# Kernel optimization log

Measured on AMD Instinct MI355X. Metric: run time of the kernel, lower is better.

## Reference

```python
import jax, jax.numpy as jnp
import numpy as np

B, S, D_IN, D_OUT = 8, 4096, 1280, 1280
K1, K2, K3 = 4, 8, 40  # svd_l[1280]


def setup_inputs() -> dict:
    key = jax.random.key(0)
    kx, k1, k2, k3, kw = jax.random.split(key, 5)
    return {
        "x": jax.random.normal(kx, (B, S, D_IN), dtype=jnp.float32),
        "kron_1": jax.random.normal(k1, (K1, K1), dtype=jnp.float32),
        "kron_2": jax.random.normal(k2, (K2, K2), dtype=jnp.float32),
        "kron_3": jax.random.normal(k3, (K3, K3), dtype=jnp.float32),
        "W": jax.random.normal(kw, (D_OUT, D_IN), dtype=jnp.float32) * 0.02,
    }


def _cayley(A):
    # Q = (I - skew) @ inv(I + skew), skew = 0.5*(A - A^T)
    n = A.shape[0]
    skew = 0.5 * (A - A.T)
    I = jnp.eye(n, dtype=A.dtype)
    return (I - skew) @ jnp.linalg.inv(I + skew)


def reference(x, kron_1, kron_2, kron_3, W):
    q1 = _cayley(kron_1)
    q2 = _cayley(kron_2)
    q3 = _cayley(kron_3)
    # R: [in, in] nested Kronecker of the three orthogonal factors
    R = jnp.kron(jnp.kron(q1, q2), q3)
    # filt = (R @ W^T)^T = W @ R^T  -> [out, in]
    filt = (R @ W.T).T
    # linear(x, filt): x @ filt^T  -> [B, S, out]
    return jnp.einsum("bsi,oi->bso", x, filt)
```

## Files before the change

### kernel.cpp

```cpp
#include <hip/hip_runtime.h>
#include <stdint.h>

#define D_IN 1280

typedef __attribute__((ext_vector_type(8))) short s16x8;
typedef __attribute__((ext_vector_type(4))) float f32x4;
typedef __attribute__((ext_vector_type(4))) unsigned int u32x4;

__device__ __forceinline__ unsigned short f2bf(float f) {
  union { float f; unsigned u; } v;
  v.f = f;
  unsigned u = v.u;
  return (unsigned short)((u + 0x7fffu + ((u >> 16) & 1u)) >> 16);
}

__device__ __forceinline__ unsigned int cvtpk(float lo, float hi) {
  unsigned int r;
  asm("v_cvt_pk_bf16_f32 %0, %1, %2" : "=v"(r) : "v"(lo), "v"(hi));
  return r;
}

__device__ __forceinline__ void gload_lds16(const void* g, void* l) {
  __builtin_amdgcn_global_load_lds(
      (const __attribute__((address_space(1))) void*)g,
      (__attribute__((address_space(3))) void*)l, 16, 0, 0);
}

__global__ void cayley_kernel(const float* __restrict__ A1,
                              const float* __restrict__ A2,
                              const float* __restrict__ A3,
                              float* __restrict__ qws) {
  const int which = blockIdx.x;
  const float* __restrict__ A = which == 0 ? A1 : (which == 1 ? A2 : A3);
  float* __restrict__ Q = which == 0 ? qws : (which == 1 ? qws + 16 : qws + 80);
  const int n = which == 0 ? 4 : (which == 1 ? 8 : 40);
  const int t = threadIdx.x;

  __shared__ float aug[40][80];
  __shared__ float Nm[40][40];
  __shared__ float fac[40];

  for (int idx = t; idx < n * n; idx += 256) {
    int i = idx / n, j = idx % n;
    float s = 0.5f * (A[i * n + j] - A[j * n + i]);
    float eye = (i == j) ? 1.0f : 0.0f;
    aug[i][j] = eye + s;
    aug[i][n + j] = eye;
    Nm[i][j] = eye - s;
  }
  __syncthreads();

  for (int p = 0; p < n; ++p) {
    const float d = aug[p][p];
    if (t < n) fac[t] = (t == p) ? 0.0f : aug[t][p];
    __syncthreads();
    const float inv = 1.0f / d;
    if (t < 2 * n) aug[p][t] *= inv;
    __syncthreads();
    for (int idx = t; idx < n * 2 * n; idx += 256) {
      int i = idx / (2 * n), j = idx % (2 * n);
      aug[i][j] -= fac[i] * aug[p][j];
    }
    __syncthreads();
  }

  for (int idx = t; idx < n * n; idx += 256) {
    int i = idx / n, j = idx % n;
    float acc = 0.0f;
    for (int k = 0; k < n; ++k) acc += Nm[i][k] * aug[k][n + j];
    Q[i * n + j] = acc;
  }
}

#define FROWS 4
__global__ __launch_bounds__(320) void filt_kernel(const float* __restrict__ W,
                                                   const float* __restrict__ qws,
                                                   unsigned short* __restrict__ filt) {
  __shared__ float q1s[16];
  __shared__ float q2s[64];
  __shared__ float w[FROWS][D_IN];
  __shared__ float t1[FROWS][D_IN];
  __shared__ float t2[FROWS][D_IN];
  const int t = threadIdx.x;
  const int ob = blockIdx.x * FROWS;

  if (t < 16) q1s[t] = qws[t];
  if (t < 64) q2s[t] = qws[16 + t];

  const int i3 = t % 40;
  const int g = t / 40;
  float q3c[40];
#pragma unroll
  for (int j3 = 0; j3 < 40; ++j3) q3c[j3] = qws[80 + i3 * 40 + j3];

  for (int k = t; k < FROWS * 320; k += 320) {
    int r = k / 320, c = k % 320;
    ((float4*)w[r])[c] = ((const float4*)(W + (size_t)(ob + r) * D_IN))[c];
  }
  __syncthreads();

#pragma unroll
  for (int kk = 0; kk < 16; ++kk) {
    const int item = g * 16 + kk;
    const int r = item >> 5;
    const int b = (item & 31) * 40;
    float s = 0.0f;
#pragma unroll
    for (int j3 = 0; j3 < 40; ++j3) s += w[r][b + j3] * q3c[j3];
    t1[r][b + i3] = s;
  }
  __syncthreads();

  for (int e = t; e < FROWS * D_IN; e += 320) {
    const int r = e / D_IN;
    const int i = e - r * D_IN;
    const int ii3 = i % 40;
    const int i2 = (i / 40) & 7;
    const int j1 = i / 320;
    float s = 0.0f;
#pragma unroll
    for (int j2 = 0; j2 < 8; ++j2) s += q2s[i2 * 8 + j2] * t1[r][j1 * 320 + j2 * 40 + ii3];
    t2[r][i] = s;
  }
  __syncthreads();

  for (int e = t; e < FROWS * D_IN; e += 320) {
    const int r = e / D_IN;
    const int i = e - r * D_IN;
    const int lo = i % 320;
    const int i1 = i / 320;
    float s = 0.0f;
#pragma unroll
    for (int j1 = 0; j1 < 4; ++j1) s += q1s[i1 * 4 + j1] * t2[r][j1 * 320 + lo];
    filt[(size_t)(ob + r) * D_IN + i] = f2bf(s);
  }
}

__global__ __launch_bounds__(256) void cvt_kernel(const float* __restrict__ x,
                                                  unsigned short* __restrict__ xb) {
  const size_t i = ((size_t)blockIdx.x * 256 + threadIdx.x) * 8;
  float4 a = *(const float4*)(x + i);
  float4 b = *(const float4*)(x + i + 4);
  u32x4 p;
  p[0] = cvtpk(a.x, a.y);
  p[1] = cvtpk(a.z, a.w);
  p[2] = cvtpk(b.x, b.y);
  p[3] = cvtpk(b.z, b.w);
  *(u32x4*)(xb + i) = p;
}

__global__ __launch_bounds__(512, 2) void gemm8p_kernel(
    const unsigned short* __restrict__ xb,
    const unsigned short* __restrict__ filt,
    float* __restrict__ out) {
  __shared__ short As[2][2][128][64];
  __shared__ short Bs[2][2][128][64];

  const int t = threadIdx.x;
  const int lane = t & 63;
  const int wave = t >> 6;
  const int wr = wave >> 2;
  const int wc = wave & 3;
  const int hb = wc >> 1;
  const int nloc = (wc & 1) * 64;

  const int nwg = gridDim.x;
  const int bid = blockIdx.x;
  const int wg = (bid & 7) * (nwg >> 3) + (bid >> 3);
  const int mt = wg / 5;
  const int nt = wg % 5;
  const int mbase = mt * 256;
  const int nbase = nt * 256;

  f32x4 acc[8][4];
#pragma unroll
  for (int m = 0; m < 8; ++m)
#pragma unroll
    for (int n = 0; n < 4; ++n) acc[m][n] = 0.0f;

  const int tr = t >> 3;
  const int scol = (((t & 7) ^ (tr & 7)) << 3);
  const int pslot = (t & 7) << 3;
  const unsigned short* __restrict__ abase = xb + (size_t)mbase * D_IN + scol;
  const unsigned short* __restrict__ bbase = filt + (size_t)nbase * D_IN + scol;

#define STAGE_A(P, H, KT)                                                     \
  {                                                                           \
    _Pragma("unroll")                                                         \
    for (int q = 0; q < 2; ++q)                                               \
      gload_lds16(abase + (size_t)((H)*128 + q * 64 + tr) * D_IN + (KT)*64,   \
                  (void*)&As[P][H][q * 64 + tr][pslot]);                      \
  }
#define STAGE_B(P, H, KT)                                                     \
  {                                                                           \
    _Pragma("unroll")                                                         \
    for (int q = 0; q < 2; ++q)                                               \
      gload_lds16(bbase + (size_t)((H)*128 + q * 64 + tr) * D_IN + (KT)*64,   \
                  (void*)&Bs[P][H][q * 64 + tr][pslot]);                      \
  }

  const int lr = lane & 15;
  const int hk = lane >> 4;
  const int c0 = ((hk ^ (lr & 7)) << 3);
  const int c1 = c0 ^ 32;

#define BAR asm volatile("s_barrier" ::: "memory")
#define LGKM0 asm volatile("s_waitcnt lgkmcnt(0)" ::: "memory")

  STAGE_A(0, 0, 0); STAGE_A(0, 1, 0);
  STAGE_B(0, 0, 0); STAGE_B(0, 1, 0);
  STAGE_A(1, 0, 1);
  asm volatile("s_waitcnt vmcnt(2)" ::: "memory");
  BAR;

  s16x8 aLo[8], aHi[8], bLo[4], bHi[4];

#pragma unroll 2
  for (int j = 0; j < 20; ++j) {
    const int d = j & 1;

#pragma unroll
    for (int m = 0; m < 4; ++m) {
      aLo[m * 2 + 0] = *(const s16x8*)&As[d][wr][m * 16 + lr][c0];
      aLo[m * 2 + 1] = *(const s16x8*)&As[d][wr][m * 16 + lr][c1];
    }
#pragma unroll
    for (int n = 0; n < 2; ++n) {
      bLo[n * 2 + 0] = *(const s16x8*)&Bs[d][hb][nloc + n * 16 + lr][c0];
      bLo[n * 2 + 1] = *(const s16x8*)&Bs[d][hb][nloc + n * 16 + lr][c1];
    }
    if (j < 19) STAGE_A(d ^ 1, 1, j + 1);
    BAR; LGKM0;
    __builtin_amdgcn_s_setprio(1);
#pragma unroll
    for (int m = 0; m < 4; ++m)
#pragma unroll
      for (int n = 0; n < 2; ++n)
#pragma unroll
        for (int kk = 0; kk < 2; ++kk)
          acc[m][n] = __builtin_amdgcn_mfma_f32_16x16x32_bf16(
              aLo[m * 2 + kk], bLo[n * 2 + kk], acc[m][n], 0, 0, 0);
    __builtin_amdgcn_s_setprio(0);
    BAR;

#pragma unroll
    for (int n = 0; n < 2; ++n) {
      bHi[n * 2 + 0] = *(const s16x8*)&Bs[d][hb][nloc + (n + 2) * 16 + lr][c0];
      bHi[n * 2 + 1] = *(const s16x8*)&Bs[d][hb][nloc + (n + 2) * 16 + lr][c1];
    }
    if (j < 19) STAGE_B(d ^ 1, 0, j + 1);
    BAR; LGKM0;
    __builtin_amdgcn_s_setprio(1);
#pragma unroll
    for (int m = 0; m < 4; ++m)
#pragma unroll
      for (int n = 0; n < 2; ++n)
#pragma unroll
        for (int kk = 0; kk < 2; ++kk)
          acc[m][n + 2] = __builtin_amdgcn_mfma_f32_16x16x32_bf16(
              aLo[m * 2 + kk], bHi[n * 2 + kk], acc[m][n + 2], 0, 0, 0);
    __builtin_amdgcn_s_setprio(0);
    BAR;

#pragma unroll
    for (int m = 0; m < 4; ++m) {
      aHi[m * 2 + 0] = *(const s16x8*)&As[d][wr][(m + 4) * 16 + lr][c0];
      aHi[m * 2 + 1] = *(const s16x8*)&As[d][wr][(m + 4) * 16 + lr][c1];
    }
    if (j < 19) STAGE_B(d ^ 1, 1, j + 1);
    BAR; LGKM0;
    __builtin_amdgcn_s_setprio(1);
#pragma unroll
    for (int m = 0; m < 4; ++m)
#pragma unroll
      for (int n = 0; n < 2; ++n)
#pragma unroll
        for (int kk = 0; kk < 2; ++kk)
          acc[m + 4][n + 2] = __builtin_amdgcn_mfma_f32_16x16x32_bf16(
              aHi[m * 2 + kk], bHi[n * 2 + kk], acc[m + 4][n + 2], 0, 0, 0);
    __builtin_amdgcn_s_setprio(0);
    BAR;

    if (j < 18) STAGE_A(d, 0, j + 2);
    BAR;
    __builtin_amdgcn_s_setprio(1);
#pragma unroll
    for (int m = 0; m < 4; ++m)
#pragma unroll
      for (int n = 0; n < 2; ++n)
#pragma unroll
        for (int kk = 0; kk < 2; ++kk)
          acc[m + 4][n] = __builtin_amdgcn_mfma_f32_16x16x32_bf16(
              aHi[m * 2 + kk], bLo[n * 2 + kk], acc[m + 4][n], 0, 0, 0);
    __builtin_amdgcn_s_setprio(0);
    if (j <= 17)      asm volatile("s_waitcnt vmcnt(2)" ::: "memory");
    else if (j == 18) asm volatile("s_waitcnt vmcnt(0)" ::: "memory");
    BAR;
  }
#undef STAGE_A
#undef STAGE_B
#undef BAR
#undef LGKM0

  const int orow = (lane >> 4) << 2;
  const int ocol = lane & 15;
#pragma unroll
  for (int m = 0; m < 8; ++m) {
#pragma unroll
    for (int r = 0; r < 4; ++r) {
      float* cp = out + (size_t)(mbase + wr * 128 + m * 16 + orow + r) * D_IN +
                  nbase + wc * 64 + ocol;
#pragma unroll
      for (int n = 0; n < 4; ++n) cp[n * 16] = acc[m][n][r];
    }
  }
}

__global__ __launch_bounds__(256) void gemm_fb_kernel(const float* __restrict__ x,
                                                      const unsigned short* __restrict__ filt,
                                                      float* __restrict__ out) {
  __shared__ short As[128][32];
  __shared__ short Bs[128][32];

  const int t = threadIdx.x;
  const int lane = t & 63;
  const int wave = t >> 6;
  const int wr = wave >> 1;
  const int wc = wave & 1;

  const int nwg = gridDim.x;
  const int bid = blockIdx.x;
  const int wg = (bid & 7) * (nwg >> 3) + (bid >> 3);
  const int mt = wg / 10;
  const int nt = wg % 10;
  const int mbase = mt * 128;
  const int nbase = nt * 128;

  f32x4 acc[4][4];
#pragma unroll
  for (int m = 0; m < 4; ++m)
#pragma unroll
    for (int n = 0; n < 4; ++n) acc[m][n] = 0.0f;

  const int ar = t >> 1;
  const int ac = (t & 1) << 4;
  const float* __restrict__ asrc = x + (size_t)(mbase + ar) * D_IN + ac;

  const int br = t >> 2;
  const int bc = (t & 3) << 3;
  const unsigned short* __restrict__ bsrc0 = filt + (size_t)(nbase + br) * D_IN + bc;
  const unsigned short* __restrict__ bsrc1 = filt + (size_t)(nbase + br + 64) * D_IN + bc;
  short* bdst0 = &Bs[br][bc];
  short* bdst1 = &Bs[br + 64][bc];

  const int lr = lane & 15;
  const int lk = (lane >> 4) << 3;

  for (int kt = 0; kt < D_IN; kt += 32) {
    gload_lds16(bsrc0 + kt, bdst0);
    gload_lds16(bsrc1 + kt, bdst1);

    const float* src = asrc + kt;
    float4 f0 = *(const float4*)(src + 0);
    float4 f1 = *(const float4*)(src + 4);
    float4 f2 = *(const float4*)(src + 8);
    float4 f3 = *(const float4*)(src + 12);
    u32x4 p0, p1;
    p0[0] = cvtpk(f0.x, f0.y); p0[1] = cvtpk(f0.z, f0.w);
    p0[2] = cvtpk(f1.x, f1.y); p0[3] = cvtpk(f1.z, f1.w);
    p1[0] = cvtpk(f2.x, f2.y); p1[1] = cvtpk(f2.z, f2.w);
    p1[2] = cvtpk(f3.x, f3.y); p1[3] = cvtpk(f3.z, f3.w);
    *(u32x4*)&As[ar][ac] = p0;
    *(u32x4*)&As[ar][ac + 16] = p1;

    __syncthreads();

    s16x8 a[4], b[4];
#pragma unroll
    for (int m = 0; m < 4; ++m)
      a[m] = *(const s16x8*)&As[wr * 64 + m * 16 + lr][lk];
#pragma unroll
    for (int n = 0; n < 4; ++n)
      b[n] = *(const s16x8*)&Bs[wc * 64 + n * 16 + lr][lk];
#pragma unroll
    for (int m = 0; m < 4; ++m)
#pragma unroll
      for (int n = 0; n < 4; ++n)
        acc[m][n] = __builtin_amdgcn_mfma_f32_16x16x32_bf16(a[m], b[n], acc[m][n], 0, 0, 0);

    __syncthreads();
  }

  const int orow = (lane >> 4) << 2;
  const int ocol = lane & 15;
#pragma unroll
  for (int m = 0; m < 4; ++m) {
#pragma unroll
    for (int r = 0; r < 4; ++r) {
      float* cp = out + (size_t)(mbase + wr * 64 + m * 16 + orow + r) * D_IN +
                  nbase + wc * 64 + ocol;
#pragma unroll
      for (int n = 0; n < 4; ++n) cp[n * 16] = acc[m][n][r];
    }
  }
}

extern "C" void kernel_launch(void* const* d_in, const int* in_sizes, int n_in,
                              void* d_out, int out_size, void* d_ws, size_t ws_size,
                              hipStream_t stream) {
  (void)in_sizes; (void)n_in; (void)out_size;
  const float* x = (const float*)d_in[0];
  const float* k1 = (const float*)d_in[1];
  const float* k2 = (const float*)d_in[2];
  const float* k3 = (const float*)d_in[3];
  const float* W = (const float*)d_in[4];
  float* out = (float*)d_out;

  float* qws = (float*)d_ws;
  unsigned short* filt = (unsigned short*)((char*)d_ws + 8192);
  unsigned short* xb = (unsigned short*)((char*)d_ws + (4u << 20));
  const size_t need = (4ull << 20) + (size_t)32768 * D_IN * 2;

  cayley_kernel<<<3, 256, 0, stream>>>(k1, k2, k3, qws);
  filt_kernel<<<D_IN / FROWS, 320, 0, stream>>>(W, qws, filt);

  if (ws_size >= need) {
    cvt_kernel<<<20480, 256, 0, stream>>>(x, xb);
    gemm8p_kernel<<<640, 512, 0, stream>>>(xb, filt, out);
  } else {
    gemm_fb_kernel<<<2560, 256, 0, stream>>>(x, filt, out);
  }
}
```

Before: 268.3 us.

## Fuse fp32-to-bf16 conversion of x into the GEMM A-tile staging

New measurement: 288.8 us. 7.7% more time.

```diff
diff --git a/kernel.cpp b/kernel.cpp
--- a/kernel.cpp
+++ b/kernel.cpp
@@ -136,21 +136,8 @@
   }
 }
 
-__global__ __launch_bounds__(256) void cvt_kernel(const float* __restrict__ x,
-                                                  unsigned short* __restrict__ xb) {
-  const size_t i = ((size_t)blockIdx.x * 256 + threadIdx.x) * 8;
-  float4 a = *(const float4*)(x + i);
-  float4 b = *(const float4*)(x + i + 4);
-  u32x4 p;
-  p[0] = cvtpk(a.x, a.y);
-  p[1] = cvtpk(a.z, a.w);
-  p[2] = cvtpk(b.x, b.y);
-  p[3] = cvtpk(b.z, b.w);
-  *(u32x4*)(xb + i) = p;
-}
-
 __global__ __launch_bounds__(512, 2) void gemm8p_kernel(
-    const unsigned short* __restrict__ xb,
+    const float* __restrict__ x,
     const unsigned short* __restrict__ filt,
     float* __restrict__ out) {
   __shared__ short As[2][2][128][64];
@@ -181,16 +168,8 @@
   const int tr = t >> 3;
   const int scol = (((t & 7) ^ (tr & 7)) << 3);
   const int pslot = (t & 7) << 3;
-  const unsigned short* __restrict__ abase = xb + (size_t)mbase * D_IN + scol;
   const unsigned short* __restrict__ bbase = filt + (size_t)nbase * D_IN + scol;
 
-#define STAGE_A(P, H, KT)                                                     \
-  {                                                                           \
-    _Pragma("unroll")                                                         \
-    for (int q = 0; q < 2; ++q)                                               \
-      gload_lds16(abase + (size_t)((H)*128 + q * 64 + tr) * D_IN + (KT)*64,   \
-                  (void*)&As[P][H][q * 64 + tr][pslot]);                      \
-  }
 #define STAGE_B(P, H, KT)                                                     \
   {                                                                           \
     _Pragma("unroll")                                                         \
@@ -199,6 +178,32 @@
                   (void*)&Bs[P][H][q * 64 + tr][pslot]);                      \
   }
 
+  const int ar = t >> 2;
+  const int acol = (t & 3) * 16;
+  const int as0 = (t & 3) * 2;
+  const int am = ar & 7;
+  const float* __restrict__ a0base = x + (size_t)(mbase + ar) * D_IN + acol;
+  const float* __restrict__ a1base = x + (size_t)(mbase + 128 + ar) * D_IN + acol;
+
+#define LOAD_A(LA, BASE, KT)                                                  \
+  {                                                                           \
+    const float* _s = (BASE) + (KT)*64;                                       \
+    LA[0] = *(const f32x4*)(_s + 0);                                          \
+    LA[1] = *(const f32x4*)(_s + 4);                                          \
+    LA[2] = *(const f32x4*)(_s + 8);                                          \
+    LA[3] = *(const f32x4*)(_s + 12);                                         \
+  }
+#define WRITE_A(P, H, LA)                                                     \
+  {                                                                           \
+    u32x4 _w0, _w1;                                                           \
+    _w0[0] = cvtpk(LA[0][0], LA[0][1]); _w0[1] = cvtpk(LA[0][2], LA[0][3]);   \
+    _w0[2] = cvtpk(LA[1][0], LA[1][1]); _w0[3] = cvtpk(LA[1][2], LA[1][3]);   \
+    _w1[0] = cvtpk(LA[2][0], LA[2][1]); _w1[1] = cvtpk(LA[2][2], LA[2][3]);   \
+    _w1[2] = cvtpk(LA[3][0], LA[3][1]); _w1[3] = cvtpk(LA[3][2], LA[3][3]);   \
+    *(u32x4*)&As[P][H][ar][(as0 ^ am) << 3] = _w0;                            \
+    *(u32x4*)&As[P][H][ar][((as0 + 1) ^ am) << 3] = _w1;                      \
+  }
+
   const int lr = lane & 15;
   const int hk = lane >> 4;
   const int c0 = ((hk ^ (lr & 7)) << 3);
@@ -207,11 +212,15 @@
 #define BAR asm volatile("s_barrier" ::: "memory")
 #define LGKM0 asm volatile("s_waitcnt lgkmcnt(0)" ::: "memory")
 
-  STAGE_A(0, 0, 0); STAGE_A(0, 1, 0);
+  f32x4 la0[4], la1[4];
+
+  LOAD_A(la0, a0base, 0);
+  LOAD_A(la1, a1base, 0);
   STAGE_B(0, 0, 0); STAGE_B(0, 1, 0);
-  STAGE_A(1, 0, 1);
-  asm volatile("s_waitcnt vmcnt(2)" ::: "memory");
-  BAR;
+  asm volatile("s_waitcnt vmcnt(0)" ::: "memory");
+  WRITE_A(0, 0, la0);
+  WRITE_A(0, 1, la1);
+  LGKM0; BAR;
 
   s16x8 aLo[8], aHi[8], bLo[4], bHi[4];
 
@@ -229,7 +238,7 @@
       bLo[n * 2 + 0] = *(const s16x8*)&Bs[d][hb][nloc + n * 16 + lr][c0];
       bLo[n * 2 + 1] = *(const s16x8*)&Bs[d][hb][nloc + n * 16 + lr][c1];
     }
-    if (j < 19) STAGE_A(d ^ 1, 1, j + 1);
+    if (j < 19) LOAD_A(la0, a0base, j + 1);
     BAR; LGKM0;
     __builtin_amdgcn_s_setprio(1);
 #pragma unroll
@@ -248,7 +257,10 @@
       bHi[n * 2 + 0] = *(const s16x8*)&Bs[d][hb][nloc + (n + 2) * 16 + lr][c0];
       bHi[n * 2 + 1] = *(const s16x8*)&Bs[d][hb][nloc + (n + 2) * 16 + lr][c1];
     }
-    if (j < 19) STAGE_B(d ^ 1, 0, j + 1);
+    if (j < 19) {
+      STAGE_B(d ^ 1, 0, j + 1);
+      LOAD_A(la1, a1base, j + 1);
+    }
     BAR; LGKM0;
     __builtin_amdgcn_s_setprio(1);
 #pragma unroll
@@ -281,7 +293,6 @@
     __builtin_amdgcn_s_setprio(0);
     BAR;
 
-    if (j < 18) STAGE_A(d, 0, j + 2);
     BAR;
     __builtin_amdgcn_s_setprio(1);
 #pragma unroll
@@ -293,12 +304,17 @@
           acc[m + 4][n] = __builtin_amdgcn_mfma_f32_16x16x32_bf16(
               aHi[m * 2 + kk], bLo[n * 2 + kk], acc[m + 4][n], 0, 0, 0);
     __builtin_amdgcn_s_setprio(0);
-    if (j <= 17)      asm volatile("s_waitcnt vmcnt(2)" ::: "memory");
-    else if (j == 18) asm volatile("s_waitcnt vmcnt(0)" ::: "memory");
-    BAR;
-  }
-#undef STAGE_A
+    if (j < 19) {
+      asm volatile("s_waitcnt vmcnt(0)" ::: "memory");
+      WRITE_A(d ^ 1, 0, la0);
+      WRITE_A(d ^ 1, 1, la1);
+      LGKM0;
+    }
+    BAR;
+  }
 #undef STAGE_B
+#undef LOAD_A
+#undef WRITE_A
 #undef BAR
 #undef LGKM0
 
@@ -316,99 +332,10 @@
   }
 }
 
-__global__ __launch_bounds__(256) void gemm_fb_kernel(const float* __restrict__ x,
-                                                      const unsigned short* __restrict__ filt,
-                                                      float* __restrict__ out) {
-  __shared__ short As[128][32];
-  __shared__ short Bs[128][32];
-
-  const int t = threadIdx.x;
-  const int lane = t & 63;
-  const int wave = t >> 6;
-  const int wr = wave >> 1;
-  const int wc = wave & 1;
-
-  const int nwg = gridDim.x;
-  const int bid = blockIdx.x;
-  const int wg = (bid & 7) * (nwg >> 3) + (bid >> 3);
-  const int mt = wg / 10;
-  const int nt = wg % 10;
-  const int mbase = mt * 128;
-  const int nbase = nt * 128;
-
-  f32x4 acc[4][4];
-#pragma unroll
-  for (int m = 0; m < 4; ++m)
-#pragma unroll
-    for (int n = 0; n < 4; ++n) acc[m][n] = 0.0f;
-
-  const int ar = t >> 1;
-  const int ac = (t & 1) << 4;
-  const float* __restrict__ asrc = x + (size_t)(mbase + ar) * D_IN + ac;
-
-  const int br = t >> 2;
-  const int bc = (t & 3) << 3;
-  const unsigned short* __restrict__ bsrc0 = filt + (size_t)(nbase + br) * D_IN + bc;
-  const unsigned short* __restrict__ bsrc1 = filt + (size_t)(nbase + br + 64) * D_IN + bc;
-  short* bdst0 = &Bs[br][bc];
-  short* bdst1 = &Bs[br + 64][bc];
-
-  const int lr = lane & 15;
-  const int lk = (lane >> 4) << 3;
-
-  for (int kt = 0; kt < D_IN; kt += 32) {
-    gload_lds16(bsrc0 + kt, bdst0);
-    gload_lds16(bsrc1 + kt, bdst1);
-
-    const float* src = asrc + kt;
-    float4 f0 = *(const float4*)(src + 0);
-    float4 f1 = *(const float4*)(src + 4);
-    float4 f2 = *(const float4*)(src + 8);
-    float4 f3 = *(const float4*)(src + 12);
-    u32x4 p0, p1;
-    p0[0] = cvtpk(f0.x, f0.y); p0[1] = cvtpk(f0.z, f0.w);
-    p0[2] = cvtpk(f1.x, f1.y); p0[3] = cvtpk(f1.z, f1.w);
-    p1[0] = cvtpk(f2.x, f2.y); p1[1] = cvtpk(f2.z, f2.w);
-    p1[2] = cvtpk(f3.x, f3.y); p1[3] = cvtpk(f3.z, f3.w);
-    *(u32x4*)&As[ar][ac] = p0;
-    *(u32x4*)&As[ar][ac + 16] = p1;
-
-    __syncthreads();
-
-    s16x8 a[4], b[4];
-#pragma unroll
-    for (int m = 0; m < 4; ++m)
-      a[m] = *(const s16x8*)&As[wr * 64 + m * 16 + lr][lk];
-#pragma unroll
-    for (int n = 0; n < 4; ++n)
-      b[n] = *(const s16x8*)&Bs[wc * 64 + n * 16 + lr][lk];
-#pragma unroll
-    for (int m = 0; m < 4; ++m)
-#pragma unroll
-      for (int n = 0; n < 4; ++n)
-        acc[m][n] = __builtin_amdgcn_mfma_f32_16x16x32_bf16(a[m], b[n], acc[m][n], 0, 0, 0);
-
-    __syncthreads();
-  }
-
-  const int orow = (lane >> 4) << 2;
-  const int ocol = lane & 15;
-#pragma unroll
-  for (int m = 0; m < 4; ++m) {
-#pragma unroll
-    for (int r = 0; r < 4; ++r) {
-      float* cp = out + (size_t)(mbase + wr * 64 + m * 16 + orow + r) * D_IN +
-                  nbase + wc * 64 + ocol;
-#pragma unroll
-      for (int n = 0; n < 4; ++n) cp[n * 16] = acc[m][n][r];
-    }
-  }
-}
-
 extern "C" void kernel_launch(void* const* d_in, const int* in_sizes, int n_in,
                               void* d_out, int out_size, void* d_ws, size_t ws_size,
                               hipStream_t stream) {
-  (void)in_sizes; (void)n_in; (void)out_size;
+  (void)in_sizes; (void)n_in; (void)out_size; (void)ws_size;
   const float* x = (const float*)d_in[0];
   const float* k1 = (const float*)d_in[1];
   const float* k2 = (const float*)d_in[2];
@@ -418,16 +345,8 @@
 
   float* qws = (float*)d_ws;
   unsigned short* filt = (unsigned short*)((char*)d_ws + 8192);
-  unsigned short* xb = (unsigned short*)((char*)d_ws + (4u << 20));
-  const size_t need = (4ull << 20) + (size_t)32768 * D_IN * 2;
 
   cayley_kernel<<<3, 256, 0, stream>>>(k1, k2, k3, qws);
   filt_kernel<<<D_IN / FROWS, 320, 0, stream>>>(W, qws, filt);
-
-  if (ws_size >= need) {
-    cvt_kernel<<<20480, 256, 0, stream>>>(x, xb);
-    gemm8p_kernel<<<640, 512, 0, stream>>>(xb, filt, out);
-  } else {
-    gemm_fb_kernel<<<2560, 256, 0, stream>>>(x, filt, out);
-  }
-}
+  gemm8p_kernel<<<640, 512, 0, stream>>>(x, filt, out);
+}
```

## Fuse Cayley, filter build and x-to-bf16 conversion into one prep kernel

Applied to the files above, without the earlier changes.

Measured after the change: 232.3 us (median of 2 runs). 1.15x faster.

```diff
diff --git a/kernel.cpp b/kernel.cpp
--- a/kernel.cpp
+++ b/kernel.cpp
@@ -2,6 +2,7 @@
 #include <stdint.h>
 
 #define D_IN 1280
+#define FROWS 4
 
 typedef __attribute__((ext_vector_type(8))) short s16x8;
 typedef __attribute__((ext_vector_type(4))) float f32x4;
@@ -26,77 +27,90 @@
       (__attribute__((address_space(3))) void*)l, 16, 0, 0);
 }
 
-__global__ void cayley_kernel(const float* __restrict__ A1,
-                              const float* __restrict__ A2,
-                              const float* __restrict__ A3,
-                              float* __restrict__ qws) {
-  const int which = blockIdx.x;
-  const float* __restrict__ A = which == 0 ? A1 : (which == 1 ? A2 : A3);
-  float* __restrict__ Q = which == 0 ? qws : (which == 1 ? qws + 16 : qws + 80);
-  const int n = which == 0 ? 4 : (which == 1 ? 8 : 40);
+__global__ __launch_bounds__(320) void prep_kernel(
+    const float* __restrict__ A1, const float* __restrict__ A2,
+    const float* __restrict__ A3, const float* __restrict__ W,
+    const float* __restrict__ x, unsigned short* __restrict__ filt,
+    unsigned short* __restrict__ xb) {
+  __shared__ __align__(16) char smem[69632];
+  const int bid = blockIdx.x;
   const int t = threadIdx.x;
 
-  __shared__ float aug[40][80];
-  __shared__ float Nm[40][40];
-  __shared__ float fac[40];
-
-  for (int idx = t; idx < n * n; idx += 256) {
-    int i = idx / n, j = idx % n;
-    float s = 0.5f * (A[i * n + j] - A[j * n + i]);
-    float eye = (i == j) ? 1.0f : 0.0f;
-    aug[i][j] = eye + s;
-    aug[i][n + j] = eye;
-    Nm[i][j] = eye - s;
-  }
-  __syncthreads();
-
-  for (int p = 0; p < n; ++p) {
-    const float d = aug[p][p];
-    if (t < n) fac[t] = (t == p) ? 0.0f : aug[t][p];
+  if (bid >= 320) {
+    const size_t stride = (size_t)2048 * 320 * 8;
+    size_t i = ((size_t)(bid - 320) * 320 + t) * 8;
+#pragma unroll
+    for (int it = 0; it < 8; ++it, i += stride) {
+      float4 a = *(const float4*)(x + i);
+      float4 b = *(const float4*)(x + i + 4);
+      u32x4 p;
+      p[0] = cvtpk(a.x, a.y); p[1] = cvtpk(a.z, a.w);
+      p[2] = cvtpk(b.x, b.y); p[3] = cvtpk(b.z, b.w);
+      *(u32x4*)(xb + i) = p;
+    }
+    return;
+  }
+
+  float (*wS)[D_IN]  = (float (*)[D_IN])(smem);
+  float (*t1S)[D_IN] = (float (*)[D_IN])(smem + 20480);
+  float (*t2S)[D_IN] = (float (*)[D_IN])(smem + 40960);
+  float (*augS)[80]  = (float (*)[80])(smem + 40960);
+  float (*NmS)[40]   = (float (*)[40])(smem + 53760);
+  float* facS        = (float*)(smem + 60160);
+  float* q1S         = (float*)(smem + 61440);
+  float* q2S         = (float*)(smem + 61504);
+  float* q3S         = (float*)(smem + 61760);
+
+  const int ob = bid * FROWS;
+
+  for (int k = t; k < FROWS * 320; k += 320) {
+    int r = k / 320, c = k % 320;
+    ((float4*)wS[r])[c] = ((const float4*)(W + (size_t)(ob + r) * D_IN))[c];
+  }
+
+  for (int which = 0; which < 3; ++which) {
+    const float* __restrict__ A = which == 0 ? A1 : (which == 1 ? A2 : A3);
+    float* qd = which == 0 ? q1S : (which == 1 ? q2S : q3S);
+    const int n = which == 0 ? 4 : (which == 1 ? 8 : 40);
+
+    for (int idx = t; idx < n * n; idx += 320) {
+      int i = idx / n, j = idx % n;
+      float s = 0.5f * (A[i * n + j] - A[j * n + i]);
+      float eye = (i == j) ? 1.0f : 0.0f;
+      augS[i][j] = eye + s;
+      augS[i][n + j] = eye;
+      NmS[i][j] = eye - s;
+    }
     __syncthreads();
-    const float inv = 1.0f / d;
-    if (t < 2 * n) aug[p][t] *= inv;
+
+    for (int p = 0; p < n; ++p) {
+      const float dv = augS[p][p];
+      if (t < n) facS[t] = (t == p) ? 0.0f : augS[t][p];
+      __syncthreads();
+      const float inv = 1.0f / dv;
+      if (t < 2 * n) augS[p][t] *= inv;
+      __syncthreads();
+      for (int idx = t; idx < n * 2 * n; idx += 320) {
+        int i = idx / (2 * n), j = idx % (2 * n);
+        augS[i][j] -= facS[i] * augS[p][j];
+      }
+      __syncthreads();
+    }
+
+    for (int idx = t; idx < n * n; idx += 320) {
+      int i = idx / n, j = idx % n;
+      float acc = 0.0f;
+      for (int k = 0; k < n; ++k) acc += NmS[i][k] * augS[k][n + j];
+      qd[i * n + j] = acc;
+    }
     __syncthreads();
-    for (int idx = t; idx < n * 2 * n; idx += 256) {
-      int i = idx / (2 * n), j = idx % (2 * n);
-      aug[i][j] -= fac[i] * aug[p][j];
-    }
-    __syncthreads();
-  }
-
-  for (int idx = t; idx < n * n; idx += 256) {
-    int i = idx / n, j = idx % n;
-    float acc = 0.0f;
-    for (int k = 0; k < n; ++k) acc += Nm[i][k] * aug[k][n + j];
-    Q[i * n + j] = acc;
-  }
-}
-
-#define FROWS 4
-__global__ __launch_bounds__(320) void filt_kernel(const float* __restrict__ W,
-                                                   const float* __restrict__ qws,
-                                                   unsigned short* __restrict__ filt) {
-  __shared__ float q1s[16];
-  __shared__ float q2s[64];
-  __shared__ float w[FROWS][D_IN];
-  __shared__ float t1[FROWS][D_IN];
-  __shared__ float t2[FROWS][D_IN];
-  const int t = threadIdx.x;
-  const int ob = blockIdx.x * FROWS;
-
-  if (t < 16) q1s[t] = qws[t];
-  if (t < 64) q2s[t] = qws[16 + t];
+  }
 
   const int i3 = t % 40;
   const int g = t / 40;
   float q3c[40];
 #pragma unroll
-  for (int j3 = 0; j3 < 40; ++j3) q3c[j3] = qws[80 + i3 * 40 + j3];
-
-  for (int k = t; k < FROWS * 320; k += 320) {
-    int r = k / 320, c = k % 320;
-    ((float4*)w[r])[c] = ((const float4*)(W + (size_t)(ob + r) * D_IN))[c];
-  }
+  for (int j3 = 0; j3 < 40; ++j3) q3c[j3] = q3S[i3 * 40 + j3];
   __syncthreads();
 
 #pragma unroll
@@ -106,8 +120,8 @@
     const int b = (item & 31) * 40;
     float s = 0.0f;
 #pragma unroll
-    for (int j3 = 0; j3 < 40; ++j3) s += w[r][b + j3] * q3c[j3];
-    t1[r][b + i3] = s;
+    for (int j3 = 0; j3 < 40; ++j3) s += wS[r][b + j3] * q3c[j3];
+    t1S[r][b + i3] = s;
   }
   __syncthreads();
 
@@ -119,8 +133,8 @@
     const int j1 = i / 320;
     float s = 0.0f;
 #pragma unroll
-    for (int j2 = 0; j2 < 8; ++j2) s += q2s[i2 * 8 + j2] * t1[r][j1 * 320 + j2 * 40 + ii3];
-    t2[r][i] = s;
+    for (int j2 = 0; j2 < 8; ++j2) s += q2S[i2 * 8 + j2] * t1S[r][j1 * 320 + j2 * 40 + ii3];
+    t2S[r][i] = s;
   }
   __syncthreads();
 
@@ -131,22 +145,9 @@
     const int i1 = i / 320;
     float s = 0.0f;
 #pragma unroll
-    for (int j1 = 0; j1 < 4; ++j1) s += q1s[i1 * 4 + j1] * t2[r][j1 * 320 + lo];
+    for (int j1 = 0; j1 < 4; ++j1) s += q1S[i1 * 4 + j1] * t2S[r][j1 * 320 + lo];
     filt[(size_t)(ob + r) * D_IN + i] = f2bf(s);
   }
-}
-
-__global__ __launch_bounds__(256) void cvt_kernel(const float* __restrict__ x,
-                                                  unsigned short* __restrict__ xb) {
-  const size_t i = ((size_t)blockIdx.x * 256 + threadIdx.x) * 8;
-  float4 a = *(const float4*)(x + i);
-  float4 b = *(const float4*)(x + i + 4);
-  u32x4 p;
-  p[0] = cvtpk(a.x, a.y);
-  p[1] = cvtpk(a.z, a.w);
-  p[2] = cvtpk(b.x, b.y);
-  p[3] = cvtpk(b.z, b.w);
-  *(u32x4*)(xb + i) = p;
 }
 
 __global__ __launch_bounds__(512, 2) void gemm8p_kernel(
@@ -416,18 +417,15 @@
   const float* W = (const float*)d_in[4];
   float* out = (float*)d_out;
 
-  float* qws = (float*)d_ws;
   unsigned short* filt = (unsigned short*)((char*)d_ws + 8192);
   unsigned short* xb = (unsigned short*)((char*)d_ws + (4u << 20));
   const size_t need = (4ull << 20) + (size_t)32768 * D_IN * 2;
 
-  cayley_kernel<<<3, 256, 0, stream>>>(k1, k2, k3, qws);
-  filt_kernel<<<D_IN / FROWS, 320, 0, stream>>>(W, qws, filt);
-
   if (ws_size >= need) {
-    cvt_kernel<<<20480, 256, 0, stream>>>(x, xb);
+    prep_kernel<<<2368, 320, 0, stream>>>(k1, k2, k3, W, x, filt, xb);
     gemm8p_kernel<<<640, 512, 0, stream>>>(xb, filt, out);
   } else {
+    prep_kernel<<<320, 320, 0, stream>>>(k1, k2, k3, W, x, filt, xb);
     gemm_fb_kernel<<<2560, 256, 0, stream>>>(x, filt, out);
   }
 }
```
